# Kernel tuning notes

Measured on AMD Instinct MI355X. Metric: run time of the kernel, lower is better.

## Reference

```python
import jax, jax.numpy as jnp
import numpy as np

N_NODES = 100000
NFEAT = 128
NHID = 128
EPS_NORM = 1e-12
EPS_BN = 1e-5


def setup_inputs() -> dict:
    key = jax.random.key(0)
    ks = jax.random.split(key, 10)
    x = jax.random.normal(ks[0], (N_NODES, NFEAT), dtype=jnp.float32)
    edge_index = jax.random.randint(ks[1], (2, 1600000), 0, N_NODES, dtype=jnp.int64)
    s1 = 1.0 / np.sqrt(NFEAT)
    s2 = 1.0 / np.sqrt(NHID)
    W_l1 = jax.random.uniform(ks[2], (NHID, NFEAT), jnp.float32, -s1, s1)
    b_l1 = jax.random.uniform(ks[3], (NHID,), jnp.float32, -s1, s1)
    W_r1 = jax.random.uniform(ks[4], (NHID, NFEAT), jnp.float32, -s1, s1)
    gamma = jnp.ones((NHID,), jnp.float32)
    beta = jnp.zeros((NHID,), jnp.float32)
    W_l2 = jax.random.uniform(ks[5], (NHID, NHID), jnp.float32, -s2, s2)
    b_l2 = jax.random.uniform(ks[6], (NHID,), jnp.float32, -s2, s2)
    W_r2 = jax.random.uniform(ks[7], (NHID, NHID), jnp.float32, -s2, s2)
    return {"x": x, "edge_index": edge_index, "W_l1": W_l1, "b_l1": b_l1,
            "W_r1": W_r1, "gamma": gamma, "beta": beta, "W_l2": W_l2,
            "b_l2": b_l2, "W_r2": W_r2}


def _sage_conv(x, src, dst, W_l, b_l, W_r):
    # mean aggregation of source-node features at destination nodes
    agg = jax.ops.segment_sum(x[src], dst, num_segments=N_NODES)  # [N, F]
    cnt = jax.ops.segment_sum(jnp.ones_like(dst, dtype=x.dtype), dst,
                              num_segments=N_NODES)
    mean = agg / jnp.maximum(cnt, 1.0)[:, None]
    out = mean @ W_l.T + b_l + x @ W_r.T
    # L2 normalize (F.normalize, p=2, dim=-1)
    nrm = jnp.sqrt(jnp.sum(out * out, axis=-1, keepdims=True))
    return out / jnp.maximum(nrm, EPS_NORM)


def reference(x, edge_index, W_l1, b_l1, W_r1, gamma, beta, W_l2, b_l2, W_r2):
    src, dst = edge_index[0], edge_index[1]
    h = _sage_conv(x, src, dst, W_l1, b_l1, W_r1)
    # transition: ReLU -> BatchNorm1d (batch stats) -> Dropout (identity/eval)
    h = jax.nn.relu(h)
    mu = jnp.mean(h, axis=0)
    var = jnp.mean((h - mu) ** 2, axis=0)
    h = (h - mu) / jnp.sqrt(var + EPS_BN) * gamma + beta
    return _sage_conv(h, src, dst, W_l2, b_l2, W_r2)
```

## Files before the change

### kernel.cpp

```cpp
#include <hip/hip_runtime.h>

typedef unsigned short u16;
typedef unsigned int   u32;

#define N_NODES 100000
#define NB_BKT 196
#define CHUNK3 8192
#define NTILES 3125
#define GGRID  512

typedef short frag8 __attribute__((ext_vector_type(8)));
typedef float f32x4 __attribute__((ext_vector_type(4)));
typedef float f32x2 __attribute__((ext_vector_type(2)));
typedef u32   u32x4 __attribute__((ext_vector_type(4)));

template <typename T>
__device__ __forceinline__ T ntload(const T* p) { return __builtin_nontemporal_load(p); }
template <typename T>
__device__ __forceinline__ void ntstore(T v, T* p) { __builtin_nontemporal_store(v, p); }

__device__ __forceinline__ float bf2f(u16 h) {
    union { u32 u; float f; } c; c.u = ((u32)h) << 16; return c.f;
}
__device__ __forceinline__ u16 f2bf(float f) {
    union { float f; u32 u; } c; c.f = f;
    u32 u = c.u;
    return (u16)((u + 0x7FFFu + ((u >> 16) & 1u)) >> 16);
}
__device__ __forceinline__ float2 bfx2(u32 u) {
    union { u32 u; float f; } lo, hi;
    lo.u = u << 16; hi.u = u & 0xFFFF0000u;
    return make_float2(lo.f, hi.f);
}
__device__ __forceinline__ u32 packbf(float a, float b) {
    return (u32)f2bf(a) | ((u32)f2bf(b) << 16);
}
__device__ __forceinline__ void accum8(float* av, u32x4 q) {
    float2 p0 = bfx2(q[0]), p1 = bfx2(q[1]), p2 = bfx2(q[2]), p3 = bfx2(q[3]);
    av[0] += p0.x; av[1] += p0.y; av[2] += p1.x; av[3] += p1.y;
    av[4] += p2.x; av[5] += p2.y; av[6] += p3.x; av[7] += p3.y;
}

__device__ __forceinline__ void gload16(const void* g, void* lds) {
    __builtin_amdgcn_global_load_lds(
        (const __attribute__((address_space(1))) unsigned int*)g,
        (__attribute__((address_space(3))) unsigned int*)lds, 16, 0, 0);
}

__device__ __forceinline__ void ldsbar() {
    asm volatile("s_waitcnt lgkmcnt(0)" ::: "memory");
    __builtin_amdgcn_s_barrier();
}

union U8 { frag8 f; u16 h[8]; };

__global__ void detect_kernel(const int* __restrict__ ei, int* __restrict__ flag, int E) {
    int any = 0;
    int lim = min(2048, 2 * E);
    for (int i = 1 + 2 * (int)threadIdx.x; i < lim; i += 128) any |= ei[i];
    unsigned long long b = __ballot(any != 0);
    if (threadIdx.x == 0) *flag = (b != 0ULL) ? 1 : 0;
}


__global__ __launch_bounds__(256) void eccnt3_kernel(const int* __restrict__ ei,
                                                     int* __restrict__ blkcnt,
                                                     const int* __restrict__ flag,
                                                     int E, int nblk) {
    __shared__ int h[NB_BKT];
    const int tid = threadIdx.x;
    for (int i = tid; i < NB_BKT; i += 256) h[i] = 0;
    __syncthreads();
    const int is32 = *flag;
    const int base = blockIdx.x * CHUNK3;
    for (int i = tid; i < CHUNK3; i += 256) {
        int e = base + i;
        if (e < E) {
            int d = is32 ? ntload(&ei[E + e]) : ntload(&ei[2 * (E + (long long)e)]);
            if ((u32)d < (u32)N_NODES) atomicAdd(&h[d >> 9], 1);
        }
    }
    __syncthreads();
    for (int i = tid; i < NB_BKT; i += 256) blkcnt[i * nblk + blockIdx.x] = h[i];
}

__global__ __launch_bounds__(256) void qscanA_kernel(const int* __restrict__ blkcnt,
                                                     int* __restrict__ qbase,
                                                     int* __restrict__ btot, int nblk) {
    __shared__ int lds[256];
    const int g = blockIdx.x;
    const int t = threadIdx.x;
    int carry = 0;
    for (int base = 0; base < nblk; base += 256) {
        const int idx = base + t;
        int v = (idx < nblk) ? blkcnt[g * nblk + idx] : 0;
        lds[t] = v;
        __syncthreads();
        for (int off = 1; off < 256; off <<= 1) {
            int x = (t >= off) ? lds[t - off] : 0;
            __syncthreads();
            lds[t] += x;
            __syncthreads();
        }
        if (idx < nblk) qbase[g * nblk + idx] = carry + lds[t] - v;
        carry += lds[255];
        __syncthreads();
    }
    if (t == 0) btot[g] = carry;
}

__global__ void qscanB_kernel(const int* __restrict__ btot, int* __restrict__ bstart) {
    __shared__ int lds[256];
    const int t = threadIdx.x;
    int v = (t < NB_BKT) ? btot[t] : 0;
    lds[t] = v;
    __syncthreads();
    for (int off = 1; off < 256; off <<= 1) {
        int x = (t >= off) ? lds[t - off] : 0;
        __syncthreads();
        lds[t] += x;
        __syncthreads();
    }
    if (t < NB_BKT) bstart[t] = lds[t] - v;
    if (t == 255) bstart[NB_BKT] = lds[255];
}

__global__ __launch_bounds__(256) void ec3_kernel(const int* __restrict__ ei,
                                                  const int* __restrict__ qbase,
                                                  const int* __restrict__ bstart,
                                                  int* __restrict__ qsrc,
                                                  int* __restrict__ qdst,
                                                  const int* __restrict__ flag,
                                                  int E, int nblk) {
    __shared__ int cur[NB_BKT];
    const int tid = threadIdx.x;
    for (int i = tid; i < NB_BKT; i += 256)
        cur[i] = qbase[i * nblk + blockIdx.x] + bstart[i];
    __syncthreads();
    const int is32 = *flag;
    const int base = blockIdx.x * CHUNK3;
    for (int i = tid; i < CHUNK3; i += 256) {
        int e = base + i;
        if (e < E) {
            int d = is32 ? ntload(&ei[E + e]) : ntload(&ei[2 * (E + (long long)e)]);
            if ((u32)d < (u32)N_NODES) {
                int s = is32 ? ntload(&ei[e]) : ntload(&ei[2 * (long long)e]);
                if ((u32)s >= (u32)N_NODES) s = 0;
                int p = atomicAdd(&cur[d >> 9], 1);
                qdst[p] = d;
                qsrc[p] = s;
            }
        }
    }
}

__global__ __launch_bounds__(256) void hist3_kernel(const int* __restrict__ qdst,
                                                    const int* __restrict__ bstart,
                                                    int* __restrict__ cnt) {
    __shared__ int h[512];
    const int g = blockIdx.x;
    const int tid = threadIdx.x;
    h[tid] = 0; h[tid + 256] = 0;
    __syncthreads();
    const int qs = bstart[g], qe = bstart[g + 1];
    for (int i = qs + tid; i < qe; i += 256)
        atomicAdd(&h[ntload(&qdst[i]) & 511], 1);
    __syncthreads();
    const int node0 = g << 9;
    if (node0 + tid < N_NODES) cnt[node0 + tid] = h[tid];
    if (node0 + 256 + tid < N_NODES) cnt[node0 + 256 + tid] = h[tid + 256];
}

__global__ void scan1_kernel(const int* __restrict__ cnt, int* __restrict__ row,
                             int* __restrict__ fill, int* __restrict__ part, int n) {
    __shared__ int lds[1024];
    int t = threadIdx.x, g = blockIdx.x * 1024 + t;
    int v = (g < n) ? cnt[g] : 0;
    lds[t] = v;
    __syncthreads();
    for (int off = 1; off < 1024; off <<= 1) {
        int x = (t >= off) ? lds[t - off] : 0;
        __syncthreads();
        lds[t] += x;
        __syncthreads();
    }
    if (g < n) { row[g] = lds[t] - v; fill[g] = lds[t]; }
    if (t == 1023) part[blockIdx.x] = lds[t];
}

__global__ void scan2_kernel(int* __restrict__ part, int nb) {
    __shared__ int lds[1024];
    int t = threadIdx.x;
    int v = (t < nb) ? part[t] : 0;
    lds[t] = v;
    __syncthreads();
    for (int off = 1; off < 1024; off <<= 1) {
        int x = (t >= off) ? lds[t - off] : 0;
        __syncthreads();
        lds[t] += x;
        __syncthreads();
    }
    if (t < nb) part[t] = lds[t] - v;
}

__global__ void scan3_kernel(int* __restrict__ row, int* __restrict__ fill,
                             const int* __restrict__ part,
                             const int* __restrict__ bstart, int n) {
    int g = blockIdx.x * 1024 + threadIdx.x;
    if (g < n) { int p = part[blockIdx.x]; row[g] += p; fill[g] += p; }
    if (g == 0) row[n] = bstart[NB_BKT];
}

__global__ __launch_bounds__(256) void scatter3_kernel(const int* __restrict__ qsrc,
                                                       const int* __restrict__ qdst,
                                                       const int* __restrict__ bstart,
                                                       const int* __restrict__ fill,
                                                       int* __restrict__ csr) {
    __shared__ int cur[512];
    const int g = blockIdx.x;
    const int tid = threadIdx.x;
    const int node0 = g << 9;
    if (node0 + tid < N_NODES) cur[tid] = fill[node0 + tid];
    if (node0 + 256 + tid < N_NODES) cur[tid + 256] = fill[node0 + 256 + tid];
    __syncthreads();
    const int qs = bstart[g], qe = bstart[g + 1];
    for (int i = qs + tid; i < qe; i += 256) {
        int d = ntload(&qdst[i]);
        int s = ntload(&qsrc[i]);
        int idx = atomicSub(&cur[d & 511], 1) - 1;
        csr[idx] = s;
    }
}

__global__ void wsplitp_kernel(const float* __restrict__ W, u16* __restrict__ hi,
                               u16* __restrict__ lo) {
    int t = blockIdx.x * 256 + threadIdx.x;
    if (t >= 2048) return;
    const int f = t >> 4, ks = (t >> 2) & 3, quad = t & 3;
    const int dst = ((f >> 4) * 4 + ks) * 512 + (quad * 16 + (f & 15)) * 8;
    const float* src = W + f * 128 + ks * 32 + quad * 8;
    U8 h, l;
#pragma unroll
    for (int j = 0; j < 8; ++j) {
        float v = src[j];
        u16 hh = f2bf(v);
        h.h[j] = hh;
        l.h[j] = f2bf(v - bf2f(hh));
    }
    *(frag8*)(hi + dst) = h.f;
    *(frag8*)(lo + dst) = l.f;
}

__global__ void xtobf_kernel(const float* __restrict__ X, u16* __restrict__ outh,
                             u16* __restrict__ outl, int n2) {
    int i = blockIdx.x * 256 + threadIdx.x;
    if (i >= n2) return;
    f32x2 v = ntload(&((const f32x2*)X)[i]);
    u16 h0 = f2bf(v[0]), h1 = f2bf(v[1]);
    ((u32*)outh)[i] = (u32)h0 | ((u32)h1 << 16);
    ((u32*)outl)[i] = (u32)f2bf(v[0] - bf2f(h0)) | ((u32)f2bf(v[1] - bf2f(h1)) << 16);
}

template <int MODE>
__global__ __launch_bounds__(256) void agg_kernel(
    const u16* __restrict__ X, const int* __restrict__ rowstart,
    const int* __restrict__ csr, u16* __restrict__ out,
    const float* __restrict__ bnp) {
    const int wid = (blockIdx.x * 256 + threadIdx.x) >> 6;
    const int lane = threadIdx.x & 63;
    const int g = lane >> 4;
    const int l = lane & 15;
    if (wid >= N_NODES) return;
    const int s = rowstart[wid];
    const int deg = rowstart[wid + 1] - s;
    const u32x4* Xv = (const u32x4*)X;
    float av[8] = {0.f, 0.f, 0.f, 0.f, 0.f, 0.f, 0.f, 0.f};
    for (int base = 0; base < deg; base += 64) {
        const int nb = min(deg - base, 64);
        const int myidx = csr[s + base + min(lane, nb - 1)];
        int c = 0;
#pragma unroll 4
        for (; c + 4 <= nb; c += 4) {
            const int idx = __shfl(myidx, c + g, 64);
            u32x4 q = Xv[(size_t)idx * 16 + l];
            accum8(av, q);
        }
        if (c < nb) {
            const int idx = __shfl(myidx, min(c + g, nb - 1), 64);
            u32x4 q = Xv[(size_t)idx * 16 + l];
            if (c + g < nb) accum8(av, q);
        }
    }
#pragma unroll
    for (int j = 0; j < 8; ++j) {
        av[j] += __shfl_xor(av[j], 16, 64);
        av[j] += __shfl_xor(av[j], 32, 64);
    }
    if (g == 0) {
        const float inv = 1.0f / (float)max(deg, 1);
#pragma unroll
        for (int j = 0; j < 8; ++j) av[j] *= inv;
        if (MODE == 1) {
            if (deg > 0) {
#pragma unroll
                for (int j = 0; j < 8; ++j)
                    av[j] = av[j] * bnp[l * 8 + j] + bnp[128 + l * 8 + j];
            } else {
#pragma unroll
                for (int j = 0; j < 8; ++j) av[j] = 0.f;
            }
        }
        u32x4 o;
        o[0] = packbf(av[0], av[1]); o[1] = packbf(av[2], av[3]);
        o[2] = packbf(av[4], av[5]); o[3] = packbf(av[6], av[7]);
        ((u32x4*)out)[(size_t)wid * 16 + l] = o;
    }
}

template <int GM>
__global__ __launch_bounds__(512, 2) void gemm_kernel(
    const u16* __restrict__ A1bf, const u16* __restrict__ A2h_,
    const u16* __restrict__ A2l_, const u16* __restrict__ Wc,
    const float* __restrict__ bias, float* __restrict__ outf,
    u16* __restrict__ outb, float* __restrict__ bnsums) {
    constexpr int NREG = (GM == 0) ? 3 : 2;
    constexpr int TB = NREG * 8192;
    constexpr int OB = (GM == 0) ? 8192 : 16384;
    __shared__ __align__(16) char bufs[2][TB];
    __shared__ __align__(16) char outbuf[OB];
    __shared__ float ssrow2[32][8];
    const int tid = threadIdx.x;
    const int lane = tid & 63;
    const int wv = tid >> 6;
    const int col = lane & 15;
    const int quad = lane >> 4;

    auto stage = [&](char* buf, int trow0) {
#pragma unroll
        for (int j = 0; j < NREG; ++j) {
            const int m = j * 8 + wv;
            const int c = m & 7;
            const int rgn = m >> 3;
            const u16* srcp = (rgn == 0) ? A1bf : (rgn == 1) ? A2h_ : A2l_;
            gload16((const char*)srcp +
                        (size_t)(trow0 + ((c >> 2) << 4) + (lane & 15)) * 256 +
                        ((c & 3) << 6) + ((lane >> 4) << 4),
                    buf + m * 1024);
        }
    };

    int cur = 0;
    stage(bufs[0], blockIdx.x * 32);
    frag8 wlh[4], wll[4], wrh[4], wrl[4];
#pragma unroll
    for (int ks = 0; ks < 4; ++ks) {
        const int wo = (wv * 4 + ks) * 512 + lane * 8;
        wlh[ks] = *(const frag8*)(Wc + wo);
        wll[ks] = *(const frag8*)(Wc + 16384 + wo);
        wrh[ks] = *(const frag8*)(Wc + 32768 + wo);
        wrl[ks] = *(const frag8*)(Wc + 49152 + wo);
    }
    const float bsv = bias[wv * 16 + col];
    float bn1 = 0.f, bn2 = 0.f;

    for (int t = blockIdx.x; t < NTILES; t += GGRID) {
        __syncthreads();
        const int tn = t + GGRID;
        if (tn < NTILES) stage(bufs[cur ^ 1], tn * 32);

        f32x4 acc[2];
        acc[0] = (f32x4){0.f, 0.f, 0.f, 0.f};
        acc[1] = (f32x4){0.f, 0.f, 0.f, 0.f};
        char* buf = bufs[cur];
#pragma unroll
        for (int ks = 0; ks < 4; ++ks) {
            frag8 a1[2], a2h[2], a2l[2];
#pragma unroll
            for (int mt = 0; mt < 2; ++mt) {
                const int fo = ((mt << 2) + ks) * 1024 + lane * 16;
                a1[mt] = *(const frag8*)(buf + fo);
                a2h[mt] = *(const frag8*)(buf + 8192 + fo);
                if (GM == 0) a2l[mt] = *(const frag8*)(buf + 16384 + fo);
            }
#pragma unroll
            for (int mt = 0; mt < 2; ++mt) {
                acc[mt] = __builtin_amdgcn_mfma_f32_16x16x32_bf16(a1[mt], wlh[ks], acc[mt], 0, 0, 0);
                acc[mt] = __builtin_amdgcn_mfma_f32_16x16x32_bf16(a1[mt], wll[ks], acc[mt], 0, 0, 0);
                acc[mt] = __builtin_amdgcn_mfma_f32_16x16x32_bf16(a2h[mt], wrh[ks], acc[mt], 0, 0, 0);
                if (GM == 0)
                    acc[mt] = __builtin_amdgcn_mfma_f32_16x16x32_bf16(a2l[mt], wrh[ks], acc[mt], 0, 0, 0);
                acc[mt] = __builtin_amdgcn_mfma_f32_16x16x32_bf16(a2h[mt], wrl[ks], acc[mt], 0, 0, 0);
            }
        }

        float tv[2][4], sq[2][4];
#pragma unroll
        for (int mt = 0; mt < 2; ++mt)
#pragma unroll
            for (int r = 0; r < 4; ++r) {
                float v = acc[mt][r] + bsv;
                tv[mt][r] = v;
                sq[mt][r] = v * v;
            }
#pragma unroll
        for (int m = 1; m <= 8; m <<= 1)
#pragma unroll
            for (int mt = 0; mt < 2; ++mt)
#pragma unroll
                for (int r = 0; r < 4; ++r) sq[mt][r] += __shfl_xor(sq[mt][r], m, 64);
        if (col == 0) {
#pragma unroll
            for (int mt = 0; mt < 2; ++mt)
#pragma unroll
                for (int r = 0; r < 4; ++r)
                    ssrow2[mt * 16 + quad * 4 + r][wv] = sq[mt][r];
        }
        ldsbar();

#pragma unroll
        for (int mt = 0; mt < 2; ++mt)
#pragma unroll
            for (int r = 0; r < 4; ++r) {
                const int rw = mt * 16 + quad * 4 + r;
                f32x4 p0 = *(const f32x4*)&ssrow2[rw][0];
                f32x4 p4 = *(const f32x4*)&ssrow2[rw][4];
                float ss = ((p0[0] + p0[1]) + (p0[2] + p0[3])) +
                           ((p4[0] + p4[1]) + (p4[2] + p4[3]));
                float inv = 1.0f / fmaxf(sqrtf(ss), 1e-12f);
                float o = tv[mt][r] * inv;
                if (GM == 0) {
                    o = fmaxf(o, 0.f);
                    bn1 += o; bn2 += o * o;
                    float po = __shfl_xor(o, 1, 64);
                    if (!(lane & 1))
                        ((u32*)outbuf)[rw * 64 + wv * 8 + (col >> 1)] = packbf(o, po);
                } else {
                    ((float*)outbuf)[rw * 128 + wv * 16 + col] = o;
                }
            }
        ldsbar();

        const size_t rowbase = (size_t)t * 32;
        if (GM == 0) {
            u32x4 v = *(const u32x4*)(outbuf + tid * 16);
            *(u32x4*)((char*)outb + rowbase * 256 + tid * 16) = v;
        } else {
            f32x4 v0 = *(const f32x4*)(outbuf + tid * 32);
            f32x4 v1 = *(const f32x4*)(outbuf + tid * 32 + 16);
            ntstore(v0, (f32x4*)((char*)outf + rowbase * 512 + tid * 32));
            ntstore(v1, (f32x4*)((char*)outf + rowbase * 512 + tid * 32 + 16));
        }
        cur ^= 1;
    }

    if (GM == 0) {
        bn1 += __shfl_xor(bn1, 16, 64); bn1 += __shfl_xor(bn1, 32, 64);
        bn2 += __shfl_xor(bn2, 16, 64); bn2 += __shfl_xor(bn2, 32, 64);
        if (lane < 16) {
            const int slot = (blockIdx.x & 7) * 256;
            atomicAdd(&bnsums[slot + wv * 16 + lane], bn1);
            atomicAdd(&bnsums[slot + 128 + wv * 16 + lane], bn2);
        }
    }
}

__global__ void bnfin_kernel(const float* __restrict__ sums, const float* __restrict__ gamma,
                             const float* __restrict__ beta, float* __restrict__ bnp) {
    int f = threadIdx.x;
    if (f >= 128) return;
    float s1 = 0.f, s2 = 0.f;
#pragma unroll
    for (int k = 0; k < 8; ++k) {
        s1 += sums[k * 256 + f];
        s2 += sums[k * 256 + 128 + f];
    }
    const float invN = 1.0f / (float)N_NODES;
    float mu = s1 * invN;
    float var = s2 * invN - mu * mu;
    float sc = gamma[f] * rsqrtf(fmaxf(var, 0.f) + 1e-5f);
    bnp[f] = sc;
    bnp[128 + f] = beta[f] - mu * sc;
}

__global__ void wprep_kernel(const float* __restrict__ Wr2, const float* __restrict__ bl2,
                             const float* __restrict__ bnp, u16* __restrict__ wh,
                             u16* __restrict__ wl, float* __restrict__ bias2p) {
    __shared__ float p[2];
    const int f = blockIdx.x;
    const int k = threadIdx.x;
    float w = Wr2[f * 128 + k];
    float contrib = w * bnp[128 + k];
    float v = w * bnp[k];
    u16 h = f2bf(v);
    const int ks = k >> 5, quad = (k >> 3) & 3, j = k & 7;
    const int dst = ((f >> 4) * 4 + ks) * 512 + (quad * 16 + (f & 15)) * 8 + j;
    wh[dst] = h;
    wl[dst] = f2bf(v - bf2f(h));
#pragma unroll
    for (int m = 1; m <= 32; m <<= 1) contrib += __shfl_xor(contrib, m, 64);
    if ((k & 63) == 0) p[k >> 6] = contrib;
    __syncthreads();
    if (k == 0) bias2p[f] = bl2[f] + p[0] + p[1];
}

extern "C" void kernel_launch(void* const* d_in, const int* in_sizes, int n_in,
                              void* d_out, int out_size, void* d_ws, size_t ws_size,
                              hipStream_t stream) {
    const int N = N_NODES;
    const int E = in_sizes[1] / 2;
    const int nblk3 = (E + CHUNK3 - 1) / CHUNK3;

    const float* x     = (const float*)d_in[0];
    const int*   ei    = (const int*)d_in[1];
    const float* Wl1   = (const float*)d_in[2];
    const float* bl1   = (const float*)d_in[3];
    const float* Wr1   = (const float*)d_in[4];
    const float* gamma = (const float*)d_in[5];
    const float* beta  = (const float*)d_in[6];
    const float* Wl2   = (const float*)d_in[7];
    const float* bl2   = (const float*)d_in[8];
    const float* Wr2   = (const float*)d_in[9];
    float* outp = (float*)d_out;

    char* ws = (char*)d_ws;
    size_t off = 0;
    auto alloc = [&](size_t b) { size_t r = off; off += (b + 255) & ~(size_t)255; return r; };
    int*   flag     = (int*)  (ws + alloc(4));
    int*   cnt      = (int*)  (ws + alloc((size_t)N * 4));
    int*   rowstart = (int*)  (ws + alloc((size_t)(N + 1) * 4));
    int*   fill     = (int*)  (ws + alloc((size_t)N * 4));
    int*   partials = (int*)  (ws + alloc(4096));
    int*   bstart   = (int*)  (ws + alloc((NB_BKT + 1) * 4));
    int*   btot     = (int*)  (ws + alloc(NB_BKT * 4));
    int*   blkcnt   = (int*)  (ws + alloc((size_t)nblk3 * NB_BKT * 4));
    int*   qbase    = (int*)  (ws + alloc((size_t)nblk3 * NB_BKT * 4));
    int*   csr      = (int*)  (ws + alloc((size_t)E * 4));
    int*   qsrc     = (int*)  (ws + alloc((size_t)E * 4));
    int*   qdst     = (int*)  (ws + alloc((size_t)E * 4));
    float* bnsums   = (float*)(ws + alloc(2048 * 4));
    float* bnp      = (float*)(ws + alloc(256 * 4));
    float* bias2p   = (float*)(ws + alloc(128 * 4));
    u16*   w1c      = (u16*)  (ws + alloc(65536 * 2));
    u16*   w2c      = (u16*)  (ws + alloc(65536 * 2));
    u16*   xh       = (u16*)  (ws + alloc((size_t)N * 128 * 2));
    u16*   xl       = (u16*)  (ws + alloc((size_t)N * 128 * 2));
    u16*   meanbf   = (u16*)  (ws + alloc((size_t)N * 128 * 2));
    u16*   rhh      = (u16*)  (ws + alloc((size_t)N * 128 * 2));

    hipMemsetAsync(bnsums, 0, 2048 * 4, stream);

    detect_kernel<<<1, 64, 0, stream>>>(ei, flag, E);
    eccnt3_kernel<<<nblk3, 256, 0, stream>>>(ei, blkcnt, flag, E, nblk3);
    qscanA_kernel<<<NB_BKT, 256, 0, stream>>>(blkcnt, qbase, btot, nblk3);
    qscanB_kernel<<<1, 256, 0, stream>>>(btot, bstart);
    ec3_kernel<<<nblk3, 256, 0, stream>>>(ei, qbase, bstart, qsrc, qdst, flag, E, nblk3);
    hist3_kernel<<<NB_BKT, 256, 0, stream>>>(qdst, bstart, cnt);
    const int nb = (N + 1023) / 1024;
    scan1_kernel<<<nb, 1024, 0, stream>>>(cnt, rowstart, fill, partials, N);
    scan2_kernel<<<1, 1024, 0, stream>>>(partials, nb);
    scan3_kernel<<<nb, 1024, 0, stream>>>(rowstart, fill, partials, bstart, N);
    scatter3_kernel<<<NB_BKT, 256, 0, stream>>>(qsrc, qdst, bstart, fill, csr);

    wsplitp_kernel<<<8, 256, 0, stream>>>(Wl1, w1c, w1c + 16384);
    wsplitp_kernel<<<8, 256, 0, stream>>>(Wr1, w1c + 32768, w1c + 49152);
    wsplitp_kernel<<<8, 256, 0, stream>>>(Wl2, w2c, w2c + 16384);
    xtobf_kernel<<<(N * 64 + 255) / 256, 256, 0, stream>>>(x, xh, xl, N * 64);

    agg_kernel<0><<<(N + 3) / 4, 256, 0, stream>>>(xh, rowstart, csr, meanbf, nullptr);
    gemm_kernel<0><<<GGRID, 512, 0, stream>>>(meanbf, xh, xl, w1c,
                                              bl1, nullptr, rhh, bnsums);
    bnfin_kernel<<<1, 128, 0, stream>>>(bnsums, gamma, beta, bnp);
    wprep_kernel<<<128, 128, 0, stream>>>(Wr2, bl2, bnp, w2c + 32768, w2c + 49152, bias2p);
    agg_kernel<1><<<(N + 3) / 4, 256, 0, stream>>>(rhh, rowstart, csr, meanbf, bnp);
    gemm_kernel<1><<<GGRID, 512, 0, stream>>>(meanbf, rhh, nullptr, w2c,
                                              bias2p, outp, nullptr, nullptr);
}
```

Before: 448.8 us.

## Drop LDS output staging in GEMM, raise occupancy, widen BN atomic slots

The GEMM kernel no longer stages its output tile through shared memory. Each lane now writes its normalized results straight to global memory as packed bf16 pairs or float2, which removes the output buffer and one barrier per tile. Launch bounds go from 2 to 4 blocks per CU, the staging address math is simplified, and the BatchNorm partial-sum atomics are spread across 64 slots instead of 8 to reduce contention. The trade-off is narrower, less coalesced global stores and the loss of nontemporal stores for the float output, plus possible register pressure under the tighter launch bound.

```diff
diff --git a/kernel.cpp b/kernel.cpp
--- a/kernel.cpp
+++ b/kernel.cpp
@@ -318,16 +318,14 @@
 }
 
 template <int GM>
-__global__ __launch_bounds__(512, 2) void gemm_kernel(
+__global__ __launch_bounds__(512, 4) void gemm_kernel(
     const u16* __restrict__ A1bf, const u16* __restrict__ A2h_,
     const u16* __restrict__ A2l_, const u16* __restrict__ Wc,
     const float* __restrict__ bias, float* __restrict__ outf,
     u16* __restrict__ outb, float* __restrict__ bnsums) {
     constexpr int NREG = (GM == 0) ? 3 : 2;
     constexpr int TB = NREG * 8192;
-    constexpr int OB = (GM == 0) ? 8192 : 16384;
-    __shared__ __align__(16) char bufs[2][TB];
-    __shared__ __align__(16) char outbuf[OB];
+    __shared__ __align__(16) char bufA[TB], bufB[TB];
     __shared__ float ssrow2[32][8];
     const int tid = threadIdx.x;
     const int lane = tid & 63;
@@ -335,22 +333,18 @@
     const int col = lane & 15;
     const int quad = lane >> 4;
 
+    const int voff = (((wv >> 2) << 4) + col) * 256 + ((wv & 3) << 6) + (quad << 4);
+
     auto stage = [&](char* buf, int trow0) {
-#pragma unroll
-        for (int j = 0; j < NREG; ++j) {
-            const int m = j * 8 + wv;
-            const int c = m & 7;
-            const int rgn = m >> 3;
-            const u16* srcp = (rgn == 0) ? A1bf : (rgn == 1) ? A2h_ : A2l_;
-            gload16((const char*)srcp +
-                        (size_t)(trow0 + ((c >> 2) << 4) + (lane & 15)) * 256 +
-                        ((c & 3) << 6) + ((lane >> 4) << 4),
-                    buf + m * 1024);
-        }
+        const size_t b = (size_t)trow0 * 256 + voff;
+        gload16((const char*)A1bf + b, buf + wv * 1024);
+        gload16((const char*)A2h_ + b, buf + 8192 + wv * 1024);
+        if (GM == 0) gload16((const char*)A2l_ + b, buf + 16384 + wv * 1024);
     };
 
-    int cur = 0;
-    stage(bufs[0], blockIdx.x * 32);
+    char* cbuf = bufA;
+    char* nbuf = bufB;
+    stage(cbuf, blockIdx.x * 32);
     frag8 wlh[4], wll[4], wrh[4], wrl[4];
 #pragma unroll
     for (int ks = 0; ks < 4; ++ks) {
@@ -363,60 +357,60 @@
     const float bsv = bias[wv * 16 + col];
     float bn1 = 0.f, bn2 = 0.f;
 
+#pragma unroll 1
     for (int t = blockIdx.x; t < NTILES; t += GGRID) {
         __syncthreads();
-        const int tn = t + GGRID;
-        if (tn < NTILES) stage(bufs[cur ^ 1], tn * 32);
-
-        f32x4 acc[2];
-        acc[0] = (f32x4){0.f, 0.f, 0.f, 0.f};
-        acc[1] = (f32x4){0.f, 0.f, 0.f, 0.f};
-        char* buf = bufs[cur];
+        if (t + GGRID < NTILES) stage(nbuf, (t + GGRID) * 32);
+
+        f32x4 acc0 = (f32x4){0.f, 0.f, 0.f, 0.f};
+        f32x4 acc1 = (f32x4){0.f, 0.f, 0.f, 0.f};
 #pragma unroll
         for (int ks = 0; ks < 4; ++ks) {
-            frag8 a1[2], a2h[2], a2l[2];
-#pragma unroll
-            for (int mt = 0; mt < 2; ++mt) {
-                const int fo = ((mt << 2) + ks) * 1024 + lane * 16;
-                a1[mt] = *(const frag8*)(buf + fo);
-                a2h[mt] = *(const frag8*)(buf + 8192 + fo);
-                if (GM == 0) a2l[mt] = *(const frag8*)(buf + 16384 + fo);
+            const int fo = ks * 1024 + lane * 16;
+            frag8 a10 = *(const frag8*)(cbuf + fo);
+            frag8 a11 = *(const frag8*)(cbuf + 4096 + fo);
+            frag8 h0 = *(const frag8*)(cbuf + 8192 + fo);
+            frag8 h1 = *(const frag8*)(cbuf + 12288 + fo);
+            acc0 = __builtin_amdgcn_mfma_f32_16x16x32_bf16(a10, wlh[ks], acc0, 0, 0, 0);
+            acc0 = __builtin_amdgcn_mfma_f32_16x16x32_bf16(a10, wll[ks], acc0, 0, 0, 0);
+            acc0 = __builtin_amdgcn_mfma_f32_16x16x32_bf16(h0, wrh[ks], acc0, 0, 0, 0);
+            acc0 = __builtin_amdgcn_mfma_f32_16x16x32_bf16(h0, wrl[ks], acc0, 0, 0, 0);
+            acc1 = __builtin_amdgcn_mfma_f32_16x16x32_bf16(a11, wlh[ks], acc1, 0, 0, 0);
+            acc1 = __builtin_amdgcn_mfma_f32_16x16x32_bf16(a11, wll[ks], acc1, 0, 0, 0);
+            acc1 = __builtin_amdgcn_mfma_f32_16x16x32_bf16(h1, wrh[ks], acc1, 0, 0, 0);
+            acc1 = __builtin_amdgcn_mfma_f32_16x16x32_bf16(h1, wrl[ks], acc1, 0, 0, 0);
+            if (GM == 0) {
+                frag8 l0 = *(const frag8*)(cbuf + 16384 + fo);
+                frag8 l1 = *(const frag8*)(cbuf + 20480 + fo);
+                acc0 = __builtin_amdgcn_mfma_f32_16x16x32_bf16(l0, wrh[ks], acc0, 0, 0, 0);
+                acc1 = __builtin_amdgcn_mfma_f32_16x16x32_bf16(l1, wrh[ks], acc1, 0, 0, 0);
             }
-#pragma unroll
-            for (int mt = 0; mt < 2; ++mt) {
-                acc[mt] = __builtin_amdgcn_mfma_f32_16x16x32_bf16(a1[mt], wlh[ks], acc[mt], 0, 0, 0);
-                acc[mt] = __builtin_amdgcn_mfma_f32_16x16x32_bf16(a1[mt], wll[ks], acc[mt], 0, 0, 0);
-                acc[mt] = __builtin_amdgcn_mfma_f32_16x16x32_bf16(a2h[mt], wrh[ks], acc[mt], 0, 0, 0);
-                if (GM == 0)
-                    acc[mt] = __builtin_amdgcn_mfma_f32_16x16x32_bf16(a2l[mt], wrh[ks], acc[mt], 0, 0, 0);
-                acc[mt] = __builtin_amdgcn_mfma_f32_16x16x32_bf16(a2h[mt], wrl[ks], acc[mt], 0, 0, 0);
+        }
+
+        float sq0[4], sq1[4];
+#pragma unroll
+        for (int r = 0; r < 4; ++r) {
+            acc0[r] += bsv; acc1[r] += bsv;
+            sq0[r] = acc0[r] * acc0[r];
+            sq1[r] = acc1[r] * acc1[r];
+        }
+#pragma unroll
+        for (int m = 1; m <= 8; m <<= 1)
+#pragma unroll
+            for (int r = 0; r < 4; ++r) {
+                sq0[r] += __shfl_xor(sq0[r], m, 64);
+                sq1[r] += __shfl_xor(sq1[r], m, 64);
             }
-        }
-
-        float tv[2][4], sq[2][4];
-#pragma unroll
-        for (int mt = 0; mt < 2; ++mt)
+        if (col == 0) {
 #pragma unroll
             for (int r = 0; r < 4; ++r) {
-                float v = acc[mt][r] + bsv;
-                tv[mt][r] = v;
-                sq[mt][r] = v * v;
+                ssrow2[quad * 4 + r][wv] = sq0[r];
+                ssrow2[16 + quad * 4 + r][wv] = sq1[r];
             }
-#pragma unroll
-        for (int m = 1; m <= 8; m <<= 1)
-#pragma unroll
-            for (int mt = 0; mt < 2; ++mt)
-#pragma unroll
-                for (int r = 0; r < 4; ++r) sq[mt][r] += __shfl_xor(sq[mt][r], m, 64);
-        if (col == 0) {
-#pragma unroll
-            for (int mt = 0; mt < 2; ++mt)
-#pragma unroll
-                for (int r = 0; r < 4; ++r)
-                    ssrow2[mt * 16 + quad * 4 + r][wv] = sq[mt][r];
         }
         ldsbar();
 
+        const size_t row0 = (size_t)t * 32;
 #pragma unroll
         for (int mt = 0; mt < 2; ++mt)
 #pragma unroll
@@ -427,37 +421,30 @@
                 float ss = ((p0[0] + p0[1]) + (p0[2] + p0[3])) +
                            ((p4[0] + p4[1]) + (p4[2] + p4[3]));
                 float inv = 1.0f / fmaxf(sqrtf(ss), 1e-12f);
-                float o = tv[mt][r] * inv;
+                float o = (mt == 0 ? acc0[r] : acc1[r]) * inv;
                 if (GM == 0) {
                     o = fmaxf(o, 0.f);
                     bn1 += o; bn2 += o * o;
-                    float po = __shfl_xor(o, 1, 64);
-                    if (!(lane & 1))
-                        ((u32*)outbuf)[rw * 64 + wv * 8 + (col >> 1)] = packbf(o, po);
-                } else {
-                    ((float*)outbuf)[rw * 128 + wv * 16 + col] = o;
+                }
+                float po = __shfl_xor(o, 1, 64);
+                if (!(lane & 1)) {
+                    const size_t ridx = (row0 + rw) * 64 + wv * 8 + (col >> 1);
+                    if (GM == 0) {
+                        ((u32*)outb)[ridx] = packbf(o, po);
+                    } else {
+                        f32x2 o2; o2[0] = o; o2[1] = po;
+                        ((f32x2*)outf)[ridx] = o2;
+                    }
                 }
             }
-        ldsbar();
-
-        const size_t rowbase = (size_t)t * 32;
-        if (GM == 0) {
-            u32x4 v = *(const u32x4*)(outbuf + tid * 16);
-            *(u32x4*)((char*)outb + rowbase * 256 + tid * 16) = v;
-        } else {
-            f32x4 v0 = *(const f32x4*)(outbuf + tid * 32);
-            f32x4 v1 = *(const f32x4*)(outbuf + tid * 32 + 16);
-            ntstore(v0, (f32x4*)((char*)outf + rowbase * 512 + tid * 32));
-            ntstore(v1, (f32x4*)((char*)outf + rowbase * 512 + tid * 32 + 16));
-        }
-        cur ^= 1;
+        char* tmp = cbuf; cbuf = nbuf; nbuf = tmp;
     }
 
     if (GM == 0) {
         bn1 += __shfl_xor(bn1, 16, 64); bn1 += __shfl_xor(bn1, 32, 64);
         bn2 += __shfl_xor(bn2, 16, 64); bn2 += __shfl_xor(bn2, 32, 64);
         if (lane < 16) {
-            const int slot = (blockIdx.x & 7) * 256;
+            const int slot = (blockIdx.x & 63) * 256;
             atomicAdd(&bnsums[slot + wv * 16 + lane], bn1);
             atomicAdd(&bnsums[slot + 128 + wv * 16 + lane], bn2);
         }
@@ -470,7 +457,7 @@
     if (f >= 128) return;
     float s1 = 0.f, s2 = 0.f;
 #pragma unroll
-    for (int k = 0; k < 8; ++k) {
+    for (int k = 0; k < 64; ++k) {
         s1 += sums[k * 256 + f];
         s2 += sums[k * 256 + 128 + f];
     }
@@ -537,7 +524,7 @@
     int*   csr      = (int*)  (ws + alloc((size_t)E * 4));
     int*   qsrc     = (int*)  (ws + alloc((size_t)E * 4));
     int*   qdst     = (int*)  (ws + alloc((size_t)E * 4));
-    float* bnsums   = (float*)(ws + alloc(2048 * 4));
+    float* bnsums   = (float*)(ws + alloc(64 * 256 * 4));
     float* bnp      = (float*)(ws + alloc(256 * 4));
     float* bias2p   = (float*)(ws + alloc(128 * 4));
     u16*   w1c      = (u16*)  (ws + alloc(65536 * 2));
@@ -547,7 +534,7 @@
     u16*   meanbf   = (u16*)  (ws + alloc((size_t)N * 128 * 2));
     u16*   rhh      = (u16*)  (ws + alloc((size_t)N * 128 * 2));
 
-    hipMemsetAsync(bnsums, 0, 2048 * 4, stream);
+    hipMemsetAsync(bnsums, 0, 64 * 256 * 4, stream);
 
     detect_kernel<<<1, 64, 0, stream>>>(ei, flag, E);
     eccnt3_kernel<<<nblk3, 256, 0, stream>>>(ei, blkcnt, flag, E, nblk3);
```

Result: faster. 425.3 us (-5.2%).
